# Performance work log

Measured on AMD Instinct MI355X. Metric: run time of the kernel, lower is better.

## Reference

```python
import jax, jax.numpy as jnp
import numpy as np

SCALE = 0.08838834764831845  # 1/sqrt(128)
SOFT_CAP = 0.0
NUM_KV_HEADS = 8
RANK = 0


def setup_inputs() -> dict:
    key = jax.random.key(0)
    k0, k1, k2, k3 = jax.random.split(key, 4)
    B, H, D = 16, 32, 128
    T = 4096            # max kv length (pages per seq, page_size=1)
    P = B * T           # total pages
    q = jax.random.normal(k0, (B, H, D), jnp.float32)
    k_cache = jax.random.normal(k1, (P, 1, NUM_KV_HEADS, D), jnp.float32)
    v_cache = jax.random.normal(k2, (P, 1, NUM_KV_HEADS, D), jnp.float32)
    global_kv_lens = jax.random.randint(k3, (1, B), 1, T + 1).astype(jnp.int32)
    block_table = jnp.arange(B * T, dtype=jnp.int32).reshape(B, T)
    return {"q": q, "k_cache": k_cache, "v_cache": v_cache,
            "global_kv_lens": global_kv_lens, "block_table": block_table}


def reference(q, k_cache, v_cache, global_kv_lens, block_table):
    # Paged GQA flash-decode attention; num_ranks=1 so the Iris cross-rank
    # combine is the identity and the split-KV online softmax equals a
    # single stable softmax over the full (masked) KV length.
    kv_lens = global_kv_lens[RANK]                  # [B]
    k = k_cache[block_table, 0]                     # [B, T, KVH, D] paged gather
    v = v_cache[block_table, 0]                     # [B, T, KVH, D]
    B, H, D = q.shape
    G = H // NUM_KV_HEADS
    qh = q.reshape(B, NUM_KV_HEADS, G, D)
    s = jnp.einsum('bkgd,btkd->bkgt', qh, k) * SCALE  # [B, KVH, G, T]
    if SOFT_CAP > 0:
        s = SOFT_CAP * jnp.tanh(s / SOFT_CAP)
    T = k.shape[1]
    valid = jnp.arange(T)[None, :] < kv_lens[:, None]            # [B, T]
    s = jnp.where(valid[:, None, None, :], s, -jnp.inf)
    p = jax.nn.softmax(s, axis=-1)
    out = jnp.einsum('bkgt,btkd->bkgd', p, v).reshape(B, H, D)
    return out
```

## Files before the change

### kernel.cpp

```cpp
#include <hip/hip_runtime.h>
#include <cstdint>
#include <cstddef>


#define NB 16
#define NH 32
#define HD 128
#define NT 4096
#define NKVH 8
#define NG 4
#define NSPLIT 16
#define TILE_T 16
#define NWAVE 4
#define PART_STRIDE 520
#define SCALE_F 0.08838834764831845f
#define KVROW (NKVH * HD)

__device__ __forceinline__ void fence_sched() { __asm__ volatile("" ::: "memory"); }
#define WAIT_VM8() { __builtin_amdgcn_s_waitcnt(0x0F78); fence_sched(); }
#define WAIT_VM0() { __builtin_amdgcn_s_waitcnt(0x0F70); fence_sched(); }

__device__ __forceinline__ void glds16(const float* g, float* l) {
    __builtin_amdgcn_global_load_lds(
        (__attribute__((address_space(1))) void*)g,
        (__attribute__((address_space(3))) void*)l,
        16, 0, 0);
}

__global__ __launch_bounds__(256, 2) void attn_partial_kernel(
    const float* __restrict__ q,
    const float* __restrict__ kc,
    const float* __restrict__ vc,
    const int*   __restrict__ kv_lens,
    const int*   __restrict__ btab,
    float*       __restrict__ part)
{
    __shared__ __align__(16) float kx[NWAVE][TILE_T][HD];
    __shared__ __align__(16) float ky[NWAVE][TILE_T][HD];
    __shared__ __align__(16) float p_lds[NWAVE][TILE_T][NG];
    __shared__ __align__(16) float a_lds[NWAVE][NG];
    __shared__ __align__(16) float ml_lds[NWAVE][NG][2];

    const int bid = blockIdx.x;
    const int c   = bid % NSPLIT;
    const int kvh = (bid / NSPLIT) % NKVH;
    const int b   = bid / (NSPLIT * NKVH);
    const int tid  = threadIdx.x;
    const int w    = tid >> 6;
    const int lane = tid & 63;

    const int kv_len = kv_lens[b];
    const int clen = (kv_len + NSPLIT - 1) / NSPLIT;
    const int t0c = c * clen;
    const int t1c = min(t0c + clen, kv_len);

    float* pb = part + (size_t)bid * PART_STRIDE;

    if (t0c >= kv_len) {
        for (int i = tid; i < PART_STRIDE; i += 256)
            pb[i] = (i >= 512 && i < 516) ? -1e30f : 0.0f;
        return;
    }

    const int half = lane >> 5;
    const int cc   = lane & 31;
    const int t_s  = lane & 15;
    const int seg  = lane >> 4;
    const int t7   = t_s & 7;
    const int dp   = lane * 2;

    float4 qreg[NG][8];
    {
        const float* qb = q + ((size_t)(b * NH + kvh * NG)) * HD + seg * 32;
        #pragma unroll
        for (int g = 0; g < NG; ++g) {
            #pragma unroll
            for (int i = 0; i < 8; ++i) {
                float4 t = *((const float4*)(qb + g * HD) + i);
                qreg[g][i] = make_float4(t.x * SCALE_F, t.y * SCALE_F,
                                         t.z * SCALE_F, t.w * SCALE_F);
            }
        }
    }

    const float* kbase = kc + (size_t)kvh * HD;
    const float* vbase = vc + (size_t)kvh * HD;
    const int*   bt_b  = btab + b * NT;

    int csw[4];
    #pragma unroll
    for (int j = 0; j < 4; ++j)
        csw[j] = ((cc ^ ((2 * j + half) & 7)) << 2);

    float m_g = -1e30f, l_g = 0.0f;
    float o00=0,o01=0,o10=0,o11=0,o20=0,o21=0,o30=0,o31=0;

    int t0 = t0c + w * TILE_T;
    if (t0 < t1c) {
        int pgc[8];
        #pragma unroll
        for (int r = 0; r < 8; ++r) {
            int t = t0 + r * 2 + half;
            pgc[r] = bt_b[(t < t1c) ? t : t0c];
        }
        fence_sched();
        #pragma unroll
        for (int r = 0; r < 8; ++r)
            glds16(kbase + (size_t)pgc[r] * KVROW + csw[r & 3], &kx[w][r * 2][0]);
        fence_sched();
        #pragma unroll
        for (int r = 0; r < 8; ++r)
            glds16(vbase + (size_t)pgc[r] * KVROW + csw[r & 3], &ky[w][r * 2][0]);
        fence_sched();
    }

    for (; t0 < t1c; t0 += NWAVE * TILE_T) {
        const int t0n = t0 + NWAVE * TILE_T;
        const bool has_next = (t0n < t1c);

        WAIT_VM8();

        float s0 = 0, s1 = 0, s2 = 0, s3 = 0;
        #pragma unroll
        for (int i = 0; i < 8; ++i) {
            int pc4 = (((seg * 8 + i) ^ t7) << 2);
            float4 kk = *(const float4*)&kx[w][t_s][pc4];
            float4 q0 = qreg[0][i], q1 = qreg[1][i], q2 = qreg[2][i], q3 = qreg[3][i];
            s0 = fmaf(kk.x,q0.x,fmaf(kk.y,q0.y,fmaf(kk.z,q0.z,fmaf(kk.w,q0.w,s0))));
            s1 = fmaf(kk.x,q1.x,fmaf(kk.y,q1.y,fmaf(kk.z,q1.z,fmaf(kk.w,q1.w,s1))));
            s2 = fmaf(kk.x,q2.x,fmaf(kk.y,q2.y,fmaf(kk.z,q2.z,fmaf(kk.w,q2.w,s2))));
            s3 = fmaf(kk.x,q3.x,fmaf(kk.y,q3.y,fmaf(kk.z,q3.z,fmaf(kk.w,q3.w,s3))));
        }
        s0 += __shfl_xor(s0, 16); s0 += __shfl_xor(s0, 32);
        s1 += __shfl_xor(s1, 16); s1 += __shfl_xor(s1, 32);
        s2 += __shfl_xor(s2, 16); s2 += __shfl_xor(s2, 32);
        s3 += __shfl_xor(s3, 16); s3 += __shfl_xor(s3, 32);
        float s = (seg == 0) ? s0 : (seg == 1) ? s1 : (seg == 2) ? s2 : s3;
        if (t0 + t_s >= t1c) s = -1e30f;

        int pgn[8];
        if (has_next) {
            #pragma unroll
            for (int r = 0; r < 8; ++r) {
                int t = t0n + r * 2 + half;
                pgn[r] = bt_b[(t < t1c) ? t : t0c];
            }
        }

        float tmax = s;
        #pragma unroll
        for (int off = 1; off < 16; off <<= 1)
            tmax = fmaxf(tmax, __shfl_xor(tmax, off));
        float m_new = fmaxf(m_g, tmax);
        float alpha = __expf(m_g - m_new);
        float p     = __expf(s - m_new);
        float tsum = p;
        #pragma unroll
        for (int off = 1; off < 16; off <<= 1)
            tsum += __shfl_xor(tsum, off);
        l_g = l_g * alpha + tsum;
        m_g = m_new;

        p_lds[w][t_s][seg] = p;
        if (t_s == 0) a_lds[w][seg] = alpha;

        WAIT_VM0();

        if (has_next) {
            fence_sched();
            #pragma unroll
            for (int r = 0; r < 8; ++r)
                glds16(kbase + (size_t)pgn[r] * KVROW + csw[r & 3], &kx[w][r * 2][0]);
            fence_sched();
        }

        float a0 = a_lds[w][0], a1 = a_lds[w][1], a2 = a_lds[w][2], a3 = a_lds[w][3];
        o00 *= a0; o01 *= a0; o10 *= a1; o11 *= a1;
        o20 *= a2; o21 *= a2; o30 *= a3; o31 *= a3;
        #pragma unroll
        for (int t = 0; t < TILE_T; ++t) {
            int pc = (((lane >> 1) ^ (t & 7)) << 2) + ((lane & 1) << 1);
            float2 vv = *(const float2*)&ky[w][t][pc];
            float4 pp = *(const float4*)&p_lds[w][t][0];
            o00 = fmaf(pp.x, vv.x, o00); o01 = fmaf(pp.x, vv.y, o01);
            o10 = fmaf(pp.y, vv.x, o10); o11 = fmaf(pp.y, vv.y, o11);
            o20 = fmaf(pp.z, vv.x, o20); o21 = fmaf(pp.z, vv.y, o21);
            o30 = fmaf(pp.w, vv.x, o30); o31 = fmaf(pp.w, vv.y, o31);
        }

        if (has_next) {
            fence_sched();
            #pragma unroll
            for (int r = 0; r < 8; ++r)
                glds16(vbase + (size_t)pgn[r] * KVROW + csw[r & 3], &ky[w][r * 2][0]);
            fence_sched();
        }
    }

    {
        float* ow = &kx[w][0][0];
        ow[0 * HD + dp] = o00; ow[0 * HD + dp + 1] = o01;
        ow[1 * HD + dp] = o10; ow[1 * HD + dp + 1] = o11;
        ow[2 * HD + dp] = o20; ow[2 * HD + dp + 1] = o21;
        ow[3 * HD + dp] = o30; ow[3 * HD + dp + 1] = o31;
        if (t_s == 0) { ml_lds[w][seg][0] = m_g; ml_lds[w][seg][1] = l_g; }
    }
    __syncthreads();

    {
        int g  = tid >> 6;
        int d2 = (tid & 63) * 2;
        float M = fmaxf(fmaxf(ml_lds[0][g][0], ml_lds[1][g][0]),
                        fmaxf(ml_lds[2][g][0], ml_lds[3][g][0]));
        float L = 0.0f, O0 = 0.0f, O1 = 0.0f;
        #pragma unroll
        for (int wv = 0; wv < NWAVE; ++wv) {
            float sc = __expf(ml_lds[wv][g][0] - M);
            L  += ml_lds[wv][g][1] * sc;
            const float* owv = &kx[wv][0][0];
            O0 += owv[g * HD + d2]     * sc;
            O1 += owv[g * HD + d2 + 1] * sc;
        }
        pb[g * HD + d2]     = O0;
        pb[g * HD + d2 + 1] = O1;
        if ((tid & 63) == 0) { pb[512 + g] = M; pb[516 + g] = L; }
    }
}

__global__ __launch_bounds__(256) void attn_combine_kernel(
    const float* __restrict__ part, float* __restrict__ out)
{
    const int bid = blockIdx.x;
    const int tid = threadIdx.x;
    const int g  = tid >> 6;
    const int d2 = (tid & 63) * 2;
    const int b   = bid / NKVH;
    const int kvh = bid % NKVH;
    const float* pb = part + (size_t)bid * NSPLIT * PART_STRIDE;

    float M = -1e30f;
    #pragma unroll
    for (int cc = 0; cc < NSPLIT; ++cc)
        M = fmaxf(M, pb[cc * PART_STRIDE + 512 + g]);
    float L = 0.0f, O0 = 0.0f, O1 = 0.0f;
    #pragma unroll
    for (int cc = 0; cc < NSPLIT; ++cc) {
        float mc = pb[cc * PART_STRIDE + 512 + g];
        float sc = __expf(mc - M);
        L  += pb[cc * PART_STRIDE + 516 + g] * sc;
        O0 += pb[cc * PART_STRIDE + g * HD + d2]     * sc;
        O1 += pb[cc * PART_STRIDE + g * HD + d2 + 1] * sc;
    }
    float inv = 1.0f / L;
    const int h = kvh * NG + g;
    out[((size_t)b * NH + h) * HD + d2]     = O0 * inv;
    out[((size_t)b * NH + h) * HD + d2 + 1] = O1 * inv;
}

extern "C" void kernel_launch(void* const* d_in, const int* in_sizes, int n_in,
                              void* d_out, int out_size, void* d_ws, size_t ws_size,
                              hipStream_t stream)
{
    const float* q   = (const float*)d_in[0];
    const float* kc  = (const float*)d_in[1];
    const float* vc  = (const float*)d_in[2];
    const int*   kvl = (const int*)d_in[3];
    const int*   bt  = (const int*)d_in[4];
    float* part = (float*)d_ws;

    attn_partial_kernel<<<NB * NKVH * NSPLIT, 256, 0, stream>>>(q, kc, vc, kvl, bt, part);
    attn_combine_kernel<<<NB * NKVH, 256, 0, stream>>>(part, (float*)d_out);
}
```

Baseline: 467.8 us.

## Process all KV heads per block with full-row page loads and 64 splits

Restructures the partial kernel so each 512-thread block covers all 8 KV heads of one batch, one wave per head. Each page's full 4 KB K and V row is loaded contiguously into double-buffered LDS tiles of 4 tokens, synchronised across the block. The split count rises from 16 to 64 per sequence, and the combine kernel now reduces 64 partials with vectorized loads. The intent is more contiguous, better-coalesced page fetches and more parallelism across CUs. The cost is a block-wide barrier every 4 tokens and a larger partial buffer.

Result: slower. 486.2 us (+3.9%).

```diff
diff --git a/kernel.cpp b/kernel.cpp
--- a/kernel.cpp
+++ b/kernel.cpp
@@ -9,15 +9,13 @@
 #define NT 4096
 #define NKVH 8
 #define NG 4
-#define NSPLIT 16
-#define TILE_T 16
-#define NWAVE 4
-#define PART_STRIDE 520
+#define NSPL 64
+#define TT 4
+#define PART_STRIDE 4160
 #define SCALE_F 0.08838834764831845f
-#define KVROW (NKVH * HD)
+#define KVROW 1024
 
 __device__ __forceinline__ void fence_sched() { __asm__ volatile("" ::: "memory"); }
-#define WAIT_VM8() { __builtin_amdgcn_s_waitcnt(0x0F78); fence_sched(); }
 #define WAIT_VM0() { __builtin_amdgcn_s_waitcnt(0x0F70); fence_sched(); }
 
 __device__ __forceinline__ void glds16(const float* g, float* l) {
@@ -27,7 +25,7 @@
         16, 0, 0);
 }
 
-__global__ __launch_bounds__(256, 2) void attn_partial_kernel(
+__global__ __launch_bounds__(512, 4) void attn_partial_kernel(
     const float* __restrict__ q,
     const float* __restrict__ kc,
     const float* __restrict__ vc,
@@ -35,195 +33,149 @@
     const int*   __restrict__ btab,
     float*       __restrict__ part)
 {
-    __shared__ __align__(16) float kx[NWAVE][TILE_T][HD];
-    __shared__ __align__(16) float ky[NWAVE][TILE_T][HD];
-    __shared__ __align__(16) float p_lds[NWAVE][TILE_T][NG];
-    __shared__ __align__(16) float a_lds[NWAVE][NG];
-    __shared__ __align__(16) float ml_lds[NWAVE][NG][2];
+    __shared__ __align__(16) float kt[2][TT][KVROW];
+    __shared__ __align__(16) float vt[2][TT][KVROW];
+    __shared__ __align__(16) float p_lds[NKVH][TT][NG];
+    __shared__ float a_lds[NKVH][NG];
 
     const int bid = blockIdx.x;
-    const int c   = bid % NSPLIT;
-    const int kvh = (bid / NSPLIT) % NKVH;
-    const int b   = bid / (NSPLIT * NKVH);
-    const int tid  = threadIdx.x;
-    const int w    = tid >> 6;
+    const int c   = bid % NSPL;
+    const int b   = bid / NSPL;
+    const int tid = threadIdx.x;
+    const int w   = tid >> 6;
     const int lane = tid & 63;
 
     const int kv_len = kv_lens[b];
-    const int clen = (kv_len + NSPLIT - 1) / NSPLIT;
-    const int t0c = c * clen;
-    const int t1c = min(t0c + clen, kv_len);
+    const int clen = (kv_len + NSPL - 1) / NSPL;
+    const int t0c  = c * clen;
+    const int t1c  = min(t0c + clen, kv_len);
 
     float* pb = part + (size_t)bid * PART_STRIDE;
 
     if (t0c >= kv_len) {
-        for (int i = tid; i < PART_STRIDE; i += 256)
-            pb[i] = (i >= 512 && i < 516) ? -1e30f : 0.0f;
+        for (int i = tid; i < PART_STRIDE; i += 512)
+            pb[i] = (i >= 4096 && i < 4128) ? -1e30f : 0.0f;
         return;
     }
 
-    const int half = lane >> 5;
-    const int cc   = lane & 31;
-    const int t_s  = lane & 15;
-    const int seg  = lane >> 4;
-    const int t7   = t_s & 7;
-    const int dp   = lane * 2;
-
-    float4 qreg[NG][8];
+    const int lt = lane >> 4;
+    const int lg = (lane >> 2) & 3;
+    const int lq = lane & 3;
+
+    const int trow = w >> 1;
+    const int qb   = (w & 1) << 1;
+    const int mS  = (trow & 3) | (((lane >> 3) & 1) << 2);
+    const int lsw = ((lane ^ mS) << 2);
+
+    float4 qreg[8];
     {
-        const float* qb = q + ((size_t)(b * NH + kvh * NG)) * HD + seg * 32;
+        const float* qp = q + ((size_t)(b * NH + w * NG + lg)) * HD + (lq << 5);
         #pragma unroll
-        for (int g = 0; g < NG; ++g) {
-            #pragma unroll
-            for (int i = 0; i < 8; ++i) {
-                float4 t = *((const float4*)(qb + g * HD) + i);
-                qreg[g][i] = make_float4(t.x * SCALE_F, t.y * SCALE_F,
-                                         t.z * SCALE_F, t.w * SCALE_F);
-            }
-        }
-    }
-
-    const float* kbase = kc + (size_t)kvh * HD;
-    const float* vbase = vc + (size_t)kvh * HD;
-    const int*   bt_b  = btab + b * NT;
-
-    int csw[4];
-    #pragma unroll
-    for (int j = 0; j < 4; ++j)
-        csw[j] = ((cc ^ ((2 * j + half) & 7)) << 2);
+        for (int i = 0; i < 8; ++i) {
+            float4 t = *((const float4*)qp + i);
+            qreg[i] = make_float4(t.x * SCALE_F, t.y * SCALE_F,
+                                  t.z * SCALE_F, t.w * SCALE_F);
+        }
+    }
+
+    const int* bt_b = btab + b * NT;
+
+    const int mR = lt | ((lq & 1) << 2);
+    const float* const kqbase0 = &kt[0][lt][(w << 7) + (lq << 5)];
+    const float* const kqbase1 = &kt[1][lt][(w << 7) + (lq << 5)];
+    const int bv  = (w << 5) + (lane >> 1);
+    const int vbx = ((bv ^ (((lane >> 4) & 1) << 2)) << 2) | ((lane & 1) << 1);
 
     float m_g = -1e30f, l_g = 0.0f;
     float o00=0,o01=0,o10=0,o11=0,o20=0,o21=0,o30=0,o31=0;
 
-    int t0 = t0c + w * TILE_T;
-    if (t0 < t1c) {
-        int pgc[8];
-        #pragma unroll
-        for (int r = 0; r < 8; ++r) {
-            int t = t0 + r * 2 + half;
-            pgc[r] = bt_b[(t < t1c) ? t : t0c];
-        }
+    {
+        int tok = t0c + trow;
+        int pg = bt_b[(tok < t1c) ? tok : t0c];
+        const float* ks = kc + (size_t)pg * KVROW + lsw;
+        const float* vs = vc + (size_t)pg * KVROW + lsw;
         fence_sched();
-        #pragma unroll
-        for (int r = 0; r < 8; ++r)
-            glds16(kbase + (size_t)pgc[r] * KVROW + csw[r & 3], &kx[w][r * 2][0]);
+        glds16(ks + ((qb    ) << 8), &kt[0][trow][(qb    ) << 8]);
+        glds16(ks + ((qb + 1) << 8), &kt[0][trow][(qb + 1) << 8]);
+        glds16(vs + ((qb    ) << 8), &vt[0][trow][(qb    ) << 8]);
+        glds16(vs + ((qb + 1) << 8), &vt[0][trow][(qb + 1) << 8]);
         fence_sched();
-        #pragma unroll
-        for (int r = 0; r < 8; ++r)
-            glds16(vbase + (size_t)pgc[r] * KVROW + csw[r & 3], &ky[w][r * 2][0]);
-        fence_sched();
-    }
-
-    for (; t0 < t1c; t0 += NWAVE * TILE_T) {
-        const int t0n = t0 + NWAVE * TILE_T;
-        const bool has_next = (t0n < t1c);
-
-        WAIT_VM8();
-
-        float s0 = 0, s1 = 0, s2 = 0, s3 = 0;
+    }
+
+    int bb = 0;
+    for (int tcur = t0c; tcur < t1c; tcur += TT, bb ^= 1) {
+        const bool has_next = (tcur + TT) < t1c;
+        int pgn = 0;
+        if (has_next) {
+            int tok = tcur + TT + trow;
+            pgn = bt_b[(tok < t1c) ? tok : t0c];
+        }
+
+        WAIT_VM0();
+        __syncthreads();
+
+        if (has_next) {
+            const int nb = bb ^ 1;
+            const float* ks = kc + (size_t)pgn * KVROW + lsw;
+            const float* vs = vc + (size_t)pgn * KVROW + lsw;
+            fence_sched();
+            glds16(ks + ((qb    ) << 8), &kt[nb][trow][(qb    ) << 8]);
+            glds16(ks + ((qb + 1) << 8), &kt[nb][trow][(qb + 1) << 8]);
+            glds16(vs + ((qb    ) << 8), &vt[nb][trow][(qb    ) << 8]);
+            glds16(vs + ((qb + 1) << 8), &vt[nb][trow][(qb + 1) << 8]);
+            fence_sched();
+        }
+
+        const float* kRow = bb ? kqbase1 : kqbase0;
+        float s = 0.0f;
         #pragma unroll
         for (int i = 0; i < 8; ++i) {
-            int pc4 = (((seg * 8 + i) ^ t7) << 2);
-            float4 kk = *(const float4*)&kx[w][t_s][pc4];
-            float4 q0 = qreg[0][i], q1 = qreg[1][i], q2 = qreg[2][i], q3 = qreg[3][i];
-            s0 = fmaf(kk.x,q0.x,fmaf(kk.y,q0.y,fmaf(kk.z,q0.z,fmaf(kk.w,q0.w,s0))));
-            s1 = fmaf(kk.x,q1.x,fmaf(kk.y,q1.y,fmaf(kk.z,q1.z,fmaf(kk.w,q1.w,s1))));
-            s2 = fmaf(kk.x,q2.x,fmaf(kk.y,q2.y,fmaf(kk.z,q2.z,fmaf(kk.w,q2.w,s2))));
-            s3 = fmaf(kk.x,q3.x,fmaf(kk.y,q3.y,fmaf(kk.z,q3.z,fmaf(kk.w,q3.w,s3))));
-        }
-        s0 += __shfl_xor(s0, 16); s0 += __shfl_xor(s0, 32);
-        s1 += __shfl_xor(s1, 16); s1 += __shfl_xor(s1, 32);
-        s2 += __shfl_xor(s2, 16); s2 += __shfl_xor(s2, 32);
-        s3 += __shfl_xor(s3, 16); s3 += __shfl_xor(s3, 32);
-        float s = (seg == 0) ? s0 : (seg == 1) ? s1 : (seg == 2) ? s2 : s3;
-        if (t0 + t_s >= t1c) s = -1e30f;
-
-        int pgn[8];
-        if (has_next) {
-            #pragma unroll
-            for (int r = 0; r < 8; ++r) {
-                int t = t0n + r * 2 + half;
-                pgn[r] = bt_b[(t < t1c) ? t : t0c];
-            }
-        }
-
-        float tmax = s;
-        #pragma unroll
-        for (int off = 1; off < 16; off <<= 1)
-            tmax = fmaxf(tmax, __shfl_xor(tmax, off));
+            float4 kk = *(const float4*)(kRow + ((i ^ mR) << 2));
+            float4 qq = qreg[i];
+            s = fmaf(kk.x,qq.x, fmaf(kk.y,qq.y, fmaf(kk.z,qq.z, fmaf(kk.w,qq.w, s))));
+        }
+        s += __shfl_xor(s, 1);
+        s += __shfl_xor(s, 2);
+        if (tcur + lt >= t1c) s = -1e30f;
+
+        float tmax = fmaxf(s, __shfl_xor(s, 16));
+        tmax = fmaxf(tmax, __shfl_xor(tmax, 32));
         float m_new = fmaxf(m_g, tmax);
         float alpha = __expf(m_g - m_new);
         float p     = __expf(s - m_new);
-        float tsum = p;
-        #pragma unroll
-        for (int off = 1; off < 16; off <<= 1)
-            tsum += __shfl_xor(tsum, off);
+        float tsum  = p;
+        tsum += __shfl_xor(tsum, 16);
+        tsum += __shfl_xor(tsum, 32);
         l_g = l_g * alpha + tsum;
         m_g = m_new;
 
-        p_lds[w][t_s][seg] = p;
-        if (t_s == 0) a_lds[w][seg] = alpha;
-
-        WAIT_VM0();
-
-        if (has_next) {
-            fence_sched();
-            #pragma unroll
-            for (int r = 0; r < 8; ++r)
-                glds16(kbase + (size_t)pgn[r] * KVROW + csw[r & 3], &kx[w][r * 2][0]);
-            fence_sched();
+        if (lq == 0) {
+            p_lds[w][lt][lg] = p;
+            if (lt == 0) a_lds[w][lg] = alpha;
         }
 
         float a0 = a_lds[w][0], a1 = a_lds[w][1], a2 = a_lds[w][2], a3 = a_lds[w][3];
         o00 *= a0; o01 *= a0; o10 *= a1; o11 *= a1;
         o20 *= a2; o21 *= a2; o30 *= a3; o31 *= a3;
+        const float* vbuf = bb ? &vt[1][0][0] : &vt[0][0][0];
         #pragma unroll
-        for (int t = 0; t < TILE_T; ++t) {
-            int pc = (((lane >> 1) ^ (t & 7)) << 2) + ((lane & 1) << 1);
-            float2 vv = *(const float2*)&ky[w][t][pc];
+        for (int t = 0; t < TT; ++t) {
+            float2 vv = *(const float2*)(vbuf + t * KVROW + (vbx ^ (t << 2)));
             float4 pp = *(const float4*)&p_lds[w][t][0];
             o00 = fmaf(pp.x, vv.x, o00); o01 = fmaf(pp.x, vv.y, o01);
             o10 = fmaf(pp.y, vv.x, o10); o11 = fmaf(pp.y, vv.y, o11);
             o20 = fmaf(pp.z, vv.x, o20); o21 = fmaf(pp.z, vv.y, o21);
             o30 = fmaf(pp.w, vv.x, o30); o31 = fmaf(pp.w, vv.y, o31);
         }
-
-        if (has_next) {
-            fence_sched();
-            #pragma unroll
-            for (int r = 0; r < 8; ++r)
-                glds16(vbase + (size_t)pgn[r] * KVROW + csw[r & 3], &ky[w][r * 2][0]);
-            fence_sched();
-        }
-    }
-
-    {
-        float* ow = &kx[w][0][0];
-        ow[0 * HD + dp] = o00; ow[0 * HD + dp + 1] = o01;
-        ow[1 * HD + dp] = o10; ow[1 * HD + dp + 1] = o11;
-        ow[2 * HD + dp] = o20; ow[2 * HD + dp + 1] = o21;
-        ow[3 * HD + dp] = o30; ow[3 * HD + dp + 1] = o31;
-        if (t_s == 0) { ml_lds[w][seg][0] = m_g; ml_lds[w][seg][1] = l_g; }
-    }
-    __syncthreads();
-
-    {
-        int g  = tid >> 6;
-        int d2 = (tid & 63) * 2;
-        float M = fmaxf(fmaxf(ml_lds[0][g][0], ml_lds[1][g][0]),
-                        fmaxf(ml_lds[2][g][0], ml_lds[3][g][0]));
-        float L = 0.0f, O0 = 0.0f, O1 = 0.0f;
-        #pragma unroll
-        for (int wv = 0; wv < NWAVE; ++wv) {
-            float sc = __expf(ml_lds[wv][g][0] - M);
-            L  += ml_lds[wv][g][1] * sc;
-            const float* owv = &kx[wv][0][0];
-            O0 += owv[g * HD + d2]     * sc;
-            O1 += owv[g * HD + d2 + 1] * sc;
-        }
-        pb[g * HD + d2]     = O0;
-        pb[g * HD + d2 + 1] = O1;
-        if ((tid & 63) == 0) { pb[512 + g] = M; pb[516 + g] = L; }
+    }
+
+    *(float2*)&pb[(w * NG + 0) * HD + (lane << 1)] = make_float2(o00, o01);
+    *(float2*)&pb[(w * NG + 1) * HD + (lane << 1)] = make_float2(o10, o11);
+    *(float2*)&pb[(w * NG + 2) * HD + (lane << 1)] = make_float2(o20, o21);
+    *(float2*)&pb[(w * NG + 3) * HD + (lane << 1)] = make_float2(o30, o31);
+    if (lq == 0 && lt == 0) {
+        pb[4096 + w * NG + lg] = m_g;
+        pb[4128 + w * NG + lg] = l_g;
     }
 }
 
@@ -232,24 +184,27 @@
 {
     const int bid = blockIdx.x;
     const int tid = threadIdx.x;
-    const int g  = tid >> 6;
-    const int d2 = (tid & 63) * 2;
+    const int g   = tid >> 6;
+    const int d2  = (tid & 63) << 1;
     const int b   = bid / NKVH;
     const int kvh = bid % NKVH;
-    const float* pb = part + (size_t)bid * NSPLIT * PART_STRIDE;
+    const float* pb = part + (size_t)b * NSPL * PART_STRIDE;
+    const int mi = 4096 + kvh * NG + g;
+    const int li = 4128 + kvh * NG + g;
+    const int oi = (kvh * NG + g) * HD + d2;
 
     float M = -1e30f;
-    #pragma unroll
-    for (int cc = 0; cc < NSPLIT; ++cc)
-        M = fmaxf(M, pb[cc * PART_STRIDE + 512 + g]);
+    #pragma unroll 4
+    for (int cc = 0; cc < NSPL; ++cc)
+        M = fmaxf(M, pb[(size_t)cc * PART_STRIDE + mi]);
     float L = 0.0f, O0 = 0.0f, O1 = 0.0f;
-    #pragma unroll
-    for (int cc = 0; cc < NSPLIT; ++cc) {
-        float mc = pb[cc * PART_STRIDE + 512 + g];
-        float sc = __expf(mc - M);
-        L  += pb[cc * PART_STRIDE + 516 + g] * sc;
-        O0 += pb[cc * PART_STRIDE + g * HD + d2]     * sc;
-        O1 += pb[cc * PART_STRIDE + g * HD + d2 + 1] * sc;
+    #pragma unroll 4
+    for (int cc = 0; cc < NSPL; ++cc) {
+        const float* pc = pb + (size_t)cc * PART_STRIDE;
+        float sc = __expf(pc[mi] - M);
+        L += pc[li] * sc;
+        float2 o = *(const float2*)&pc[oi];
+        O0 = fmaf(o.x, sc, O0); O1 = fmaf(o.y, sc, O1);
     }
     float inv = 1.0f / L;
     const int h = kvh * NG + g;
@@ -268,6 +223,6 @@
     const int*   bt  = (const int*)d_in[4];
     float* part = (float*)d_ws;
 
-    attn_partial_kernel<<<NB * NKVH * NSPLIT, 256, 0, stream>>>(q, kc, vc, kvl, bt, part);
+    attn_partial_kernel<<<NB * NSPL, 512, 0, stream>>>(q, kc, vc, kvl, bt, part);
     attn_combine_kernel<<<NB * NKVH, 256, 0, stream>>>(part, (float*)d_out);
 }
```

## Load K/V directly into registers instead of async global-to-LDS staging

Applied to the files above, without the earlier changes.

Replaces the async global_load_lds staging of K and V tiles in shared memory with direct register loads. K is laid out as one token per 4-lane group and V as a float2 per lane per token. The block's page-table slice is preloaded into LDS once per block, and the score reductions are remapped to the new lane layout. This removes LDS traffic and the explicit vmcnt waits, but it adds register pressure (kreg plus 16 vreg) at 2 blocks per CU. V loads become narrow 8-byte accesses per token, and prefetch overlap now depends on compiler scheduling.

Measured after the change: 637.0 us. +36.2%, slower.

```diff
diff --git a/kernel.cpp b/kernel.cpp
--- a/kernel.cpp
+++ b/kernel.cpp
@@ -17,15 +17,6 @@
 #define KVROW (NKVH * HD)
 
 __device__ __forceinline__ void fence_sched() { __asm__ volatile("" ::: "memory"); }
-#define WAIT_VM8() { __builtin_amdgcn_s_waitcnt(0x0F78); fence_sched(); }
-#define WAIT_VM0() { __builtin_amdgcn_s_waitcnt(0x0F70); fence_sched(); }
-
-__device__ __forceinline__ void glds16(const float* g, float* l) {
-    __builtin_amdgcn_global_load_lds(
-        (__attribute__((address_space(1))) void*)g,
-        (__attribute__((address_space(3))) void*)l,
-        16, 0, 0);
-}
 
 __global__ __launch_bounds__(256, 2) void attn_partial_kernel(
     const float* __restrict__ q,
@@ -35,11 +26,11 @@
     const int*   __restrict__ btab,
     float*       __restrict__ part)
 {
-    __shared__ __align__(16) float kx[NWAVE][TILE_T][HD];
-    __shared__ __align__(16) float ky[NWAVE][TILE_T][HD];
+    __shared__ int bt_lds[256];
     __shared__ __align__(16) float p_lds[NWAVE][TILE_T][NG];
     __shared__ __align__(16) float a_lds[NWAVE][NG];
     __shared__ __align__(16) float ml_lds[NWAVE][NG][2];
+    __shared__ __align__(16) float o_lds[NWAVE][NG][HD];
 
     const int bid = blockIdx.x;
     const int c   = bid % NSPLIT;
@@ -62,55 +53,59 @@
         return;
     }
 
-    const int half = lane >> 5;
-    const int cc   = lane & 31;
-    const int t_s  = lane & 15;
-    const int seg  = lane >> 4;
-    const int t7   = t_s & 7;
-    const int dp   = lane * 2;
+    const int nchunk = t1c - t0c;
+    for (int i = tid; i < nchunk; i += 256)
+        bt_lds[i] = btab[b * NT + t0c + i];
+    __syncthreads();
+
+    const int lt = lane >> 2;
+    const int sg = lane & 3;
 
     float4 qreg[NG][8];
     {
-        const float* qb = q + ((size_t)(b * NH + kvh * NG)) * HD + seg * 32;
+        const float* qb = q + ((size_t)(b * NH + kvh * NG)) * HD + sg * 4;
         #pragma unroll
         for (int g = 0; g < NG; ++g) {
             #pragma unroll
-            for (int i = 0; i < 8; ++i) {
-                float4 t = *((const float4*)(qb + g * HD) + i);
-                qreg[g][i] = make_float4(t.x * SCALE_F, t.y * SCALE_F,
+            for (int j = 0; j < 8; ++j) {
+                float4 t = *(const float4*)(qb + g * HD + j * 16);
+                qreg[g][j] = make_float4(t.x * SCALE_F, t.y * SCALE_F,
                                          t.z * SCALE_F, t.w * SCALE_F);
             }
         }
     }
 
-    const float* kbase = kc + (size_t)kvh * HD;
-    const float* vbase = vc + (size_t)kvh * HD;
-    const int*   bt_b  = btab + b * NT;
-
-    int csw[4];
-    #pragma unroll
-    for (int j = 0; j < 4; ++j)
-        csw[j] = ((cc ^ ((2 * j + half) & 7)) << 2);
+    const float* kbase = kc + (size_t)kvh * HD + sg * 4;
+    const float* vbase = vc + (size_t)kvh * HD + 2 * lane;
 
     float m_g = -1e30f, l_g = 0.0f;
-    float o00=0,o01=0,o10=0,o11=0,o20=0,o21=0,o30=0,o31=0;
+    float o0x=0,o0y=0,o1x=0,o1y=0,o2x=0,o2y=0,o3x=0,o3y=0;
+
+    float4 kreg[8];
+    float2 vreg[TILE_T];
 
     int t0 = t0c + w * TILE_T;
+
     if (t0 < t1c) {
-        int pgc[8];
-        #pragma unroll
-        for (int r = 0; r < 8; ++r) {
-            int t = t0 + r * 2 + half;
-            pgc[r] = bt_b[(t < t1c) ? t : t0c];
-        }
+        int tokK = t0 + lt;
         fence_sched();
-        #pragma unroll
-        for (int r = 0; r < 8; ++r)
-            glds16(kbase + (size_t)pgc[r] * KVROW + csw[r & 3], &kx[w][r * 2][0]);
-        fence_sched();
-        #pragma unroll
-        for (int r = 0; r < 8; ++r)
-            glds16(vbase + (size_t)pgc[r] * KVROW + csw[r & 3], &ky[w][r * 2][0]);
+        if (tokK < t1c) {
+            const float* kp = kbase + (size_t)bt_lds[tokK - t0c] * KVROW;
+            #pragma unroll
+            for (int j = 0; j < 8; ++j)
+                kreg[j] = *(const float4*)(kp + j * 16);
+        } else {
+            #pragma unroll
+            for (int j = 0; j < 8; ++j)
+                kreg[j] = make_float4(0.f, 0.f, 0.f, 0.f);
+        }
+        #pragma unroll
+        for (int t = 0; t < TILE_T; ++t) {
+            int tok = t0 + t;
+            vreg[t] = make_float2(0.f, 0.f);
+            if (tok < t1c)
+                vreg[t] = *(const float2*)(vbase + (size_t)bt_lds[tok - t0c] * KVROW);
+        }
         fence_sched();
     }
 
@@ -118,92 +113,89 @@
         const int t0n = t0 + NWAVE * TILE_T;
         const bool has_next = (t0n < t1c);
 
-        WAIT_VM8();
-
         float s0 = 0, s1 = 0, s2 = 0, s3 = 0;
         #pragma unroll
-        for (int i = 0; i < 8; ++i) {
-            int pc4 = (((seg * 8 + i) ^ t7) << 2);
-            float4 kk = *(const float4*)&kx[w][t_s][pc4];
-            float4 q0 = qreg[0][i], q1 = qreg[1][i], q2 = qreg[2][i], q3 = qreg[3][i];
+        for (int j = 0; j < 8; ++j) {
+            float4 kk = kreg[j];
+            float4 q0 = qreg[0][j], q1 = qreg[1][j], q2 = qreg[2][j], q3 = qreg[3][j];
             s0 = fmaf(kk.x,q0.x,fmaf(kk.y,q0.y,fmaf(kk.z,q0.z,fmaf(kk.w,q0.w,s0))));
             s1 = fmaf(kk.x,q1.x,fmaf(kk.y,q1.y,fmaf(kk.z,q1.z,fmaf(kk.w,q1.w,s1))));
             s2 = fmaf(kk.x,q2.x,fmaf(kk.y,q2.y,fmaf(kk.z,q2.z,fmaf(kk.w,q2.w,s2))));
             s3 = fmaf(kk.x,q3.x,fmaf(kk.y,q3.y,fmaf(kk.z,q3.z,fmaf(kk.w,q3.w,s3))));
         }
-        s0 += __shfl_xor(s0, 16); s0 += __shfl_xor(s0, 32);
-        s1 += __shfl_xor(s1, 16); s1 += __shfl_xor(s1, 32);
-        s2 += __shfl_xor(s2, 16); s2 += __shfl_xor(s2, 32);
-        s3 += __shfl_xor(s3, 16); s3 += __shfl_xor(s3, 32);
-        float s = (seg == 0) ? s0 : (seg == 1) ? s1 : (seg == 2) ? s2 : s3;
-        if (t0 + t_s >= t1c) s = -1e30f;
-
-        int pgn[8];
+        s0 += __shfl_xor(s0, 1); s0 += __shfl_xor(s0, 2);
+        s1 += __shfl_xor(s1, 1); s1 += __shfl_xor(s1, 2);
+        s2 += __shfl_xor(s2, 1); s2 += __shfl_xor(s2, 2);
+        s3 += __shfl_xor(s3, 1); s3 += __shfl_xor(s3, 2);
+        float s = (sg == 0) ? s0 : (sg == 1) ? s1 : (sg == 2) ? s2 : s3;
+        if (t0 + lt >= t1c) s = -1e30f;
+
         if (has_next) {
-            #pragma unroll
-            for (int r = 0; r < 8; ++r) {
-                int t = t0n + r * 2 + half;
-                pgn[r] = bt_b[(t < t1c) ? t : t0c];
+            int tokK = t0n + lt;
+            fence_sched();
+            if (tokK < t1c) {
+                const float* kp = kbase + (size_t)bt_lds[tokK - t0c] * KVROW;
+                #pragma unroll
+                for (int j = 0; j < 8; ++j)
+                    kreg[j] = *(const float4*)(kp + j * 16);
+            } else {
+                #pragma unroll
+                for (int j = 0; j < 8; ++j)
+                    kreg[j] = make_float4(0.f, 0.f, 0.f, 0.f);
             }
+            fence_sched();
         }
 
         float tmax = s;
         #pragma unroll
-        for (int off = 1; off < 16; off <<= 1)
+        for (int off = 4; off < 64; off <<= 1)
             tmax = fmaxf(tmax, __shfl_xor(tmax, off));
         float m_new = fmaxf(m_g, tmax);
         float alpha = __expf(m_g - m_new);
         float p     = __expf(s - m_new);
-        float tsum = p;
-        #pragma unroll
-        for (int off = 1; off < 16; off <<= 1)
+        float tsum  = p;
+        #pragma unroll
+        for (int off = 4; off < 64; off <<= 1)
             tsum += __shfl_xor(tsum, off);
         l_g = l_g * alpha + tsum;
         m_g = m_new;
 
-        p_lds[w][t_s][seg] = p;
-        if (t_s == 0) a_lds[w][seg] = alpha;
-
-        WAIT_VM0();
+        p_lds[w][lt][sg] = p;
+        if (lt == 0) a_lds[w][sg] = alpha;
+
+        float4 aa = *(const float4*)&a_lds[w][0];
+        o0x *= aa.x; o0y *= aa.x; o1x *= aa.y; o1y *= aa.y;
+        o2x *= aa.z; o2y *= aa.z; o3x *= aa.w; o3y *= aa.w;
+        #pragma unroll
+        for (int t = 0; t < TILE_T; ++t) {
+            float4 pp = *(const float4*)&p_lds[w][t][0];
+            float2 vv = vreg[t];
+            o0x = fmaf(pp.x, vv.x, o0x); o0y = fmaf(pp.x, vv.y, o0y);
+            o1x = fmaf(pp.y, vv.x, o1x); o1y = fmaf(pp.y, vv.y, o1y);
+            o2x = fmaf(pp.z, vv.x, o2x); o2y = fmaf(pp.z, vv.y, o2y);
+            o3x = fmaf(pp.w, vv.x, o3x); o3y = fmaf(pp.w, vv.y, o3y);
+        }
 
         if (has_next) {
             fence_sched();
             #pragma unroll
-            for (int r = 0; r < 8; ++r)
-                glds16(kbase + (size_t)pgn[r] * KVROW + csw[r & 3], &kx[w][r * 2][0]);
-            fence_sched();
-        }
-
-        float a0 = a_lds[w][0], a1 = a_lds[w][1], a2 = a_lds[w][2], a3 = a_lds[w][3];
-        o00 *= a0; o01 *= a0; o10 *= a1; o11 *= a1;
-        o20 *= a2; o21 *= a2; o30 *= a3; o31 *= a3;
-        #pragma unroll
-        for (int t = 0; t < TILE_T; ++t) {
-            int pc = (((lane >> 1) ^ (t & 7)) << 2) + ((lane & 1) << 1);
-            float2 vv = *(const float2*)&ky[w][t][pc];
-            float4 pp = *(const float4*)&p_lds[w][t][0];
-            o00 = fmaf(pp.x, vv.x, o00); o01 = fmaf(pp.x, vv.y, o01);
-            o10 = fmaf(pp.y, vv.x, o10); o11 = fmaf(pp.y, vv.y, o11);
-            o20 = fmaf(pp.z, vv.x, o20); o21 = fmaf(pp.z, vv.y, o21);
-            o30 = fmaf(pp.w, vv.x, o30); o31 = fmaf(pp.w, vv.y, o31);
-        }
-
-        if (has_next) {
-            fence_sched();
-            #pragma unroll
-            for (int r = 0; r < 8; ++r)
-                glds16(vbase + (size_t)pgn[r] * KVROW + csw[r & 3], &ky[w][r * 2][0]);
+            for (int t = 0; t < TILE_T; ++t) {
+                int tok = t0n + t;
+                float2 nv = make_float2(0.f, 0.f);
+                if (tok < t1c)
+                    nv = *(const float2*)(vbase + (size_t)bt_lds[tok - t0c] * KVROW);
+                vreg[t] = nv;
+            }
             fence_sched();
         }
     }
 
     {
-        float* ow = &kx[w][0][0];
-        ow[0 * HD + dp] = o00; ow[0 * HD + dp + 1] = o01;
-        ow[1 * HD + dp] = o10; ow[1 * HD + dp + 1] = o11;
-        ow[2 * HD + dp] = o20; ow[2 * HD + dp + 1] = o21;
-        ow[3 * HD + dp] = o30; ow[3 * HD + dp + 1] = o31;
-        if (t_s == 0) { ml_lds[w][seg][0] = m_g; ml_lds[w][seg][1] = l_g; }
+        *(float2*)&o_lds[w][0][2 * lane] = make_float2(o0x, o0y);
+        *(float2*)&o_lds[w][1][2 * lane] = make_float2(o1x, o1y);
+        *(float2*)&o_lds[w][2][2 * lane] = make_float2(o2x, o2y);
+        *(float2*)&o_lds[w][3][2 * lane] = make_float2(o3x, o3y);
+        if (lt == 0) { ml_lds[w][sg][0] = m_g; ml_lds[w][sg][1] = l_g; }
     }
     __syncthreads();
 
@@ -217,9 +209,8 @@
         for (int wv = 0; wv < NWAVE; ++wv) {
             float sc = __expf(ml_lds[wv][g][0] - M);
             L  += ml_lds[wv][g][1] * sc;
-            const float* owv = &kx[wv][0][0];
-            O0 += owv[g * HD + d2]     * sc;
-            O1 += owv[g * HD + d2 + 1] * sc;
+            O0 += o_lds[wv][g][d2]     * sc;
+            O1 += o_lds[wv][g][d2 + 1] * sc;
         }
         pb[g * HD + d2]     = O0;
         pb[g * HD + d2 + 1] = O1;
```
